# Optimization experiments

Hardware: AMD Instinct MI355X
Metric: run time of the kernel (lower is better)

Reference implementation:

```python
import jax, jax.numpy as jnp
import numpy as np
from jax import lax

N = 4096
T = 8192
DT = 0.1
C_M = 1.0
E_REST = 0.0
G_M_LEAK = 5.0
I_BIAS = 0.0


def setup_inputs() -> dict:
    key = jax.random.key(0)
    i_ext_vector = jax.random.normal(key, (N, T), dtype=jnp.float32)
    return {"i_ext_vector": i_ext_vector}


def reference(i_ext_vector) -> jnp.ndarray:
    # RK2 (modified Euler) integration of leaky non-spiking neuron dynamics.
    # dv/dt = (i_bias + i_ext - (v - e_rest) * g_m_leak) / c_m
    def dvdt(v, i_ext):
        return (I_BIAS + i_ext - (v - E_REST) * G_M_LEAK) / C_M

    def step(v, i_t):
        k1 = dvdt(v, i_t)
        k2 = dvdt(v + 0.5 * DT * k1, i_t)
        v_new = v + DT * k2
        return v_new, v_new

    v0 = jnp.full((N,), E_REST, dtype=i_ext_vector.dtype)
    # scan over time: i_ext_vector is (N, T) -> scan over leading axis of (T, N)
    _, v_hist = lax.scan(step, v0, i_ext_vector.T)  # v_hist: (T, N)
    return v_hist.T  # (N, T), matches v_m_Post
```

## Files before the change

kernel.cpp:

```cpp
#include <hip/hip_runtime.h>


typedef float fx4 __attribute__((ext_vector_type(4)));

constexpr int TT    = 8192;
constexpr int BLK   = 256;
constexpr int CHUNK = 32;
constexpr int CPAD  = 36;

__global__ __launch_bounds__(BLK, 4)
void neuron_scan(const float* __restrict__ in, float* __restrict__ out) {
    __shared__ float s[BLK * CPAD];
    const float A = 0.625f;
    const float B = 0.075f;

    const int t = threadIdx.x;
    const size_t row = (size_t)blockIdx.x * TT;

    const fx4* src = (const fx4*)(in + row);
    #pragma unroll
    for (int k = 0; k < 8; ++k) {
        const int o4 = t + BLK * k;
        const fx4 val = src[o4];
        const int o = o4 << 2;
        *(fx4*)(s + (o >> 5) * CPAD + (o & 31)) = val;
    }
    __syncthreads();

    float v = 0.0f;
    #pragma unroll
    for (int w = 2; w >= 1; --w) {
        const int c = t - w;
        const fx4* p = (const fx4*)(s + (c < 0 ? 0 : c * CPAD));
        const float b = (c >= 0) ? B : 0.0f;
        #pragma unroll
        for (int q = 0; q < 8; ++q) {
            const fx4 x = p[q];
            v = fmaf(A, v, b * x.x);
            v = fmaf(A, v, b * x.y);
            v = fmaf(A, v, b * x.z);
            v = fmaf(A, v, b * x.w);
        }
    }
    __syncthreads();

    fx4* pc = (fx4*)(s + t * CPAD);
    #pragma unroll
    for (int q = 0; q < 8; ++q) {
        fx4 x = pc[q];
        v = fmaf(A, v, B * x.x); x.x = v;
        v = fmaf(A, v, B * x.y); x.y = v;
        v = fmaf(A, v, B * x.z); x.z = v;
        v = fmaf(A, v, B * x.w); x.w = v;
        pc[q] = x;
    }
    __syncthreads();

    fx4* dst = (fx4*)(out + row);
    #pragma unroll
    for (int k = 0; k < 8; ++k) {
        const int o4 = t + BLK * k;
        const int o = o4 << 2;
        const fx4 val = *(const fx4*)(s + (o >> 5) * CPAD + (o & 31));
        __builtin_nontemporal_store(val, dst + o4);
    }
}

extern "C" void kernel_launch(void* const* d_in, const int* in_sizes, int n_in,
                              void* d_out, int out_size, void* d_ws, size_t ws_size,
                              hipStream_t stream) {
    const float* in = (const float*)d_in[0];
    float* out = (float*)d_out;
    const int n_rows = in_sizes[0] / TT;
    neuron_scan<<<dim3(n_rows), dim3(BLK), 0, stream>>>(in, out);
}
```

Baseline: 231.1 us.

## Process four rows per block with register double-buffered prefetch of next row

Each block now handles four rows in a persistent loop. It prefetches the next row's input into registers while the current row is scanned in shared memory, and it replaces __syncthreads with raw LDS waitcnt plus s_barrier. The intent is to overlap global loads with compute and to cut block launch overhead. The cost is higher register pressure from holding a second buffer of 8 fx4 per thread, which may reduce occupancy, and the grid shrinks to 1024 blocks.

```diff
diff --git a/kernel.cpp b/kernel.cpp
--- a/kernel.cpp
+++ b/kernel.cpp
@@ -8,6 +8,7 @@
 constexpr int CHUNK = 32;
 constexpr int CPAD  = 36;
 
+template<int RPB>
 __global__ __launch_bounds__(BLK, 4)
 void neuron_scan(const float* __restrict__ in, float* __restrict__ out) {
     __shared__ float s[BLK * CPAD];
@@ -15,54 +16,82 @@
     const float B = 0.075f;
 
     const int t = threadIdx.x;
-    const size_t row = (size_t)blockIdx.x * TT;
+    const size_t row_stride = (size_t)gridDim.x * TT;
 
-    const fx4* src = (const fx4*)(in + row);
+    fx4 buf[2][8];
+
+    {
+        const fx4* src = (const fx4*)(in + (size_t)blockIdx.x * TT);
+        #pragma unroll
+        for (int k = 0; k < 8; ++k) buf[0][k] = src[t + BLK * k];
+    }
+
+    size_t row = (size_t)blockIdx.x * TT;
+
     #pragma unroll
-    for (int k = 0; k < 8; ++k) {
-        const int o4 = t + BLK * k;
-        const fx4 val = src[o4];
-        const int o = o4 << 2;
-        *(fx4*)(s + (o >> 5) * CPAD + (o & 31)) = val;
-    }
-    __syncthreads();
+    for (int j = 0; j < RPB; ++j) {
+        fx4* cur = buf[j & 1];
+        fx4* nxt = buf[(j + 1) & 1];
 
-    float v = 0.0f;
-    #pragma unroll
-    for (int w = 2; w >= 1; --w) {
-        const int c = t - w;
-        const fx4* p = (const fx4*)(s + (c < 0 ? 0 : c * CPAD));
-        const float b = (c >= 0) ? B : 0.0f;
+        if (j + 1 < RPB) {
+            const fx4* src = (const fx4*)(in + row + row_stride);
+            #pragma unroll
+            for (int k = 0; k < 8; ++k) nxt[k] = src[t + BLK * k];
+        }
+
+        #pragma unroll
+        for (int k = 0; k < 8; ++k) {
+            const int o = (t + BLK * k) << 2;
+            *(fx4*)(s + (o >> 5) * CPAD + (o & 31)) = cur[k];
+        }
+        asm volatile("s_waitcnt lgkmcnt(0)" ::: "memory");
+        __builtin_amdgcn_s_barrier();
+
+        float v = 0.0f;
+        #pragma unroll
+        for (int w = 2; w >= 1; --w) {
+            const int c = t - w;
+            const fx4* p = (const fx4*)(s + (c < 0 ? 0 : c * CPAD));
+            const float b = (c >= 0) ? B : 0.0f;
+            #pragma unroll
+            for (int q = 0; q < 8; ++q) {
+                const fx4 x = p[q];
+                v = fmaf(A, v, b * x.x);
+                v = fmaf(A, v, b * x.y);
+                v = fmaf(A, v, b * x.z);
+                v = fmaf(A, v, b * x.w);
+            }
+        }
+        asm volatile("s_waitcnt lgkmcnt(0)" ::: "memory");
+        __builtin_amdgcn_s_barrier();
+
+        fx4* pc = (fx4*)(s + t * CPAD);
         #pragma unroll
         for (int q = 0; q < 8; ++q) {
-            const fx4 x = p[q];
-            v = fmaf(A, v, b * x.x);
-            v = fmaf(A, v, b * x.y);
-            v = fmaf(A, v, b * x.z);
-            v = fmaf(A, v, b * x.w);
+            fx4 x = pc[q];
+            v = fmaf(A, v, B * x.x); x.x = v;
+            v = fmaf(A, v, B * x.y); x.y = v;
+            v = fmaf(A, v, B * x.z); x.z = v;
+            v = fmaf(A, v, B * x.w); x.w = v;
+            pc[q] = x;
         }
-    }
-    __syncthreads();
+        asm volatile("s_waitcnt lgkmcnt(0)" ::: "memory");
+        __builtin_amdgcn_s_barrier();
 
-    fx4* pc = (fx4*)(s + t * CPAD);
-    #pragma unroll
-    for (int q = 0; q < 8; ++q) {
-        fx4 x = pc[q];
-        v = fmaf(A, v, B * x.x); x.x = v;
-        v = fmaf(A, v, B * x.y); x.y = v;
-        v = fmaf(A, v, B * x.z); x.z = v;
-        v = fmaf(A, v, B * x.w); x.w = v;
-        pc[q] = x;
-    }
-    __syncthreads();
+        fx4* dst = (fx4*)(out + row);
+        #pragma unroll
+        for (int k = 0; k < 8; ++k) {
+            const int o4 = t + BLK * k;
+            const int o = o4 << 2;
+            const fx4 val = *(const fx4*)(s + (o >> 5) * CPAD + (o & 31));
+            __builtin_nontemporal_store(val, dst + o4);
+        }
 
-    fx4* dst = (fx4*)(out + row);
-    #pragma unroll
-    for (int k = 0; k < 8; ++k) {
-        const int o4 = t + BLK * k;
-        const int o = o4 << 2;
-        const fx4 val = *(const fx4*)(s + (o >> 5) * CPAD + (o & 31));
-        __builtin_nontemporal_store(val, dst + o4);
+        if (j + 1 < RPB) {
+            asm volatile("s_waitcnt lgkmcnt(0)" ::: "memory");
+            __builtin_amdgcn_s_barrier();
+        }
+        row += row_stride;
     }
 }
 
@@ -72,5 +101,9 @@
     const float* in = (const float*)d_in[0];
     float* out = (float*)d_out;
     const int n_rows = in_sizes[0] / TT;
-    neuron_scan<<<dim3(n_rows), dim3(BLK), 0, stream>>>(in, out);
+    if (n_rows == 4096) {
+        neuron_scan<4><<<dim3(1024), dim3(BLK), 0, stream>>>(in, out);
+    } else {
+        neuron_scan<1><<<dim3(n_rows), dim3(BLK), 0, stream>>>(in, out);
+    }
 }
```

Result: no change. 231.4 us (+0.1%).

## Split each row across two blocks with 64-step warm-up halo for second half

Applied to the files above, without the earlier changes.

Each row is now processed by two blocks, each handling half the timesteps with 16-element chunks per thread. The second-half block loads a 64-element halo before its start and uses it to warm up the recurrence, relying on the decay factor to make the truncated history negligible. Warm-up grows from 2 to 4 prior chunks, and launch bounds move to 8 blocks per CU with less shared memory per block. This raises block count and occupancy to better hide memory latency, at the cost of a small amount of redundant halo reading and compute.

```diff
diff --git a/kernel.cpp b/kernel.cpp
--- a/kernel.cpp
+++ b/kernel.cpp
@@ -5,48 +5,65 @@
 
 constexpr int TT    = 8192;
 constexpr int BLK   = 256;
-constexpr int CHUNK = 32;
-constexpr int CPAD  = 36;
+constexpr int HALF  = 4096;
+constexpr int CHUNK = 16;
+constexpr int CPAD  = 20;
+constexpr int WARM  = 4;
 
-__global__ __launch_bounds__(BLK, 4)
+__global__ __launch_bounds__(BLK, 8)
 void neuron_scan(const float* __restrict__ in, float* __restrict__ out) {
     __shared__ float s[BLK * CPAD];
     const float A = 0.625f;
     const float B = 0.075f;
 
     const int t = threadIdx.x;
-    const size_t row = (size_t)blockIdx.x * TT;
+    const int h = blockIdx.x & 1;
+    const size_t base = (size_t)(blockIdx.x >> 1) * TT + (size_t)h * HALF;
 
-    const fx4* src = (const fx4*)(in + row);
+    const fx4* src = (const fx4*)(in + base);
     #pragma unroll
-    for (int k = 0; k < 8; ++k) {
+    for (int k = 0; k < 4; ++k) {
         const int o4 = t + BLK * k;
         const fx4 val = src[o4];
         const int o = o4 << 2;
-        *(fx4*)(s + (o >> 5) * CPAD + (o & 31)) = val;
+        *(fx4*)(s + (o >> 4) * CPAD + (o & 15)) = val;
+    }
+    if (h > 0 && t < 16) {
+        const fx4 val = *(const fx4*)(in + base - 64 + 4 * t);
+        *(fx4*)(s + t * CPAD + 16) = val;
     }
     __syncthreads();
 
     float v = 0.0f;
     #pragma unroll
-    for (int w = 2; w >= 1; --w) {
+    for (int w = WARM; w >= 1; --w) {
         const int c = t - w;
-        const fx4* p = (const fx4*)(s + (c < 0 ? 0 : c * CPAD));
-        const float b = (c >= 0) ? B : 0.0f;
-        #pragma unroll
-        for (int q = 0; q < 8; ++q) {
-            const fx4 x = p[q];
-            v = fmaf(A, v, b * x.x);
-            v = fmaf(A, v, b * x.y);
-            v = fmaf(A, v, b * x.z);
-            v = fmaf(A, v, b * x.w);
+        if (c >= 0) {
+            const fx4* p = (const fx4*)(s + c * CPAD);
+            #pragma unroll
+            for (int q = 0; q < 4; ++q) {
+                const fx4 x = p[q];
+                v = fmaf(A, v, B * x.x);
+                v = fmaf(A, v, B * x.y);
+                v = fmaf(A, v, B * x.z);
+                v = fmaf(A, v, B * x.w);
+            }
+        } else if (h > 0) {
+            #pragma unroll
+            for (int q = 0; q < 4; ++q) {
+                const fx4 x = *(const fx4*)(s + (4 * (c + WARM) + q) * CPAD + 16);
+                v = fmaf(A, v, B * x.x);
+                v = fmaf(A, v, B * x.y);
+                v = fmaf(A, v, B * x.z);
+                v = fmaf(A, v, B * x.w);
+            }
         }
     }
     __syncthreads();
 
     fx4* pc = (fx4*)(s + t * CPAD);
     #pragma unroll
-    for (int q = 0; q < 8; ++q) {
+    for (int q = 0; q < 4; ++q) {
         fx4 x = pc[q];
         v = fmaf(A, v, B * x.x); x.x = v;
         v = fmaf(A, v, B * x.y); x.y = v;
@@ -56,12 +73,12 @@
     }
     __syncthreads();
 
-    fx4* dst = (fx4*)(out + row);
+    fx4* dst = (fx4*)(out + base);
     #pragma unroll
-    for (int k = 0; k < 8; ++k) {
+    for (int k = 0; k < 4; ++k) {
         const int o4 = t + BLK * k;
         const int o = o4 << 2;
-        const fx4 val = *(const fx4*)(s + (o >> 5) * CPAD + (o & 31));
+        const fx4 val = *(const fx4*)(s + (o >> 4) * CPAD + (o & 15));
         __builtin_nontemporal_store(val, dst + o4);
     }
 }
@@ -72,5 +89,5 @@
     const float* in = (const float*)d_in[0];
     float* out = (float*)d_out;
     const int n_rows = in_sizes[0] / TT;
-    neuron_scan<<<dim3(n_rows), dim3(BLK), 0, stream>>>(in, out);
+    neuron_scan<<<dim3(n_rows * 2), dim3(BLK), 0, stream>>>(in, out);
 }
```

New measurement: 228.5 us. No clear change (-1.2%).
